# Kernel optimization log

Hardware: AMD Instinct MI355X
Metric: run time of the kernel (lower is better)

The kernel has to match this reference:

```python
import jax, jax.numpy as jnp
import numpy as np

B, S, E, H = 8, 2048, 384, 6
D = E // H  # head dim = 64


def setup_inputs() -> dict:
    key = jax.random.key(0)
    ks = jax.random.split(key, 5)
    s = 1.0 / np.sqrt(E)
    return {
        "x": jax.random.normal(ks[0], (B, S, E), dtype=jnp.float32),
        "Wq": jax.random.normal(ks[1], (E, E), dtype=jnp.float32) * s,
        "Wk": jax.random.normal(ks[2], (E, E), dtype=jnp.float32) * s,
        "Wv": jax.random.normal(ks[3], (E, E), dtype=jnp.float32) * s,
        "Wo": jax.random.normal(ks[4], (E, E), dtype=jnp.float32) * s,
        "bo": jnp.zeros((E,), dtype=jnp.float32),
    }


def reference(x, Wq, Wk, Wv, Wo, bo):
    b, s, e = x.shape
    # QKV projections (torch Linear with bias=False: x @ W.T; here W stored as [in,out])
    q = (x @ Wq).reshape(b, s, H, D).transpose(0, 2, 1, 3)  # [b,h,s,d]
    k = (x @ Wk).reshape(b, s, H, D).transpose(0, 2, 1, 3)
    v = (x @ Wv).reshape(b, s, H, D).transpose(0, 2, 1, 3)
    scores = jnp.einsum("bhqd,bhkd->bhqk", q, k) / jnp.sqrt(jnp.asarray(D, x.dtype))
    causal = jnp.tril(jnp.ones((s, s), dtype=bool))
    scores = jnp.where(causal, scores, -jnp.inf)
    attn = jax.nn.softmax(scores, axis=-1)
    # NOTE: original applies dropout but then uses the PRE-dropout softmax for @V,
    # so dropout is a no-op; we faithfully omit it.
    out = jnp.einsum("bhqk,bhkd->bhqd", attn, v)  # [b,h,s,d]
    out = out.transpose(0, 2, 1, 3).reshape(b, s, e)
    return out @ Wo + bo
```

## Files before the change

kernel.cpp:

```cpp
#include <hip/hip_runtime.h>
#include <hip/hip_bf16.h>
#include <cstdint>
#include <cstddef>

typedef __attribute__((ext_vector_type(8))) short short8;
typedef __attribute__((ext_vector_type(4))) float f32x4;

#define S_LEN 2048
#define EMB 384
#define NH 6
#define HD 64
#define NB 8
#define QSCALE 0.180336880f

__device__ __forceinline__ unsigned short f2bf(float f) {
  return __builtin_bit_cast(unsigned short, __float2bfloat16(f));
}

__global__ __launch_bounds__(256) void k_prep(
    const float* __restrict__ x, unsigned short* __restrict__ xb,
    const float* __restrict__ Wq, const float* __restrict__ Wk,
    const float* __restrict__ Wv, const float* __restrict__ Wo,
    unsigned short* __restrict__ Wqt, unsigned short* __restrict__ Wkt,
    unsigned short* __restrict__ Wvt, unsigned short* __restrict__ Wot) {
  const int tid = threadIdx.x;
  if (blockIdx.x < 1536) {
    int i = blockIdx.x * 256 + tid;
    const int n4 = (NB * S_LEN * EMB) / 4;
    for (; i < n4; i += 1536 * 256) {
      const float4 v = reinterpret_cast<const float4*>(x)[i];
      ushort4 o;
      o.x = f2bf(v.x); o.y = f2bf(v.y); o.z = f2bf(v.z); o.w = f2bf(v.w);
      reinterpret_cast<ushort4*>(xb)[i] = o;
    }
  } else {
    __shared__ unsigned short Lw[64 * 66];
    const int bx2 = blockIdx.x - 1536;
    const int mat = bx2 / 36;
    const int tile = bx2 - mat * 36;
    const int k0 = (tile / 6) * 64;
    const int n0 = (tile % 6) * 64;
    const float* W = (mat == 0) ? Wq : (mat == 1) ? Wk : (mat == 2) ? Wv : Wo;
    unsigned short* Wt = (mat == 0) ? Wqt : (mat == 1) ? Wkt : (mat == 2) ? Wvt : Wot;
    const int f4 = tid & 15;
#pragma unroll
    for (int it = 0; it < 4; ++it) {
      const int kl = it * 16 + (tid >> 4);
      const float4 v = reinterpret_cast<const float4*>(W + (size_t)(k0 + kl) * EMB + n0)[f4];
      Lw[kl * 66 + f4 * 4 + 0] = f2bf(v.x);
      Lw[kl * 66 + f4 * 4 + 1] = f2bf(v.y);
      Lw[kl * 66 + f4 * 4 + 2] = f2bf(v.z);
      Lw[kl * 66 + f4 * 4 + 3] = f2bf(v.w);
    }
    __syncthreads();
    const int g = tid & 7;
#pragma unroll
    for (int it = 0; it < 2; ++it) {
      const int nl = it * 32 + (tid >> 3);
      short8 o;
#pragma unroll
      for (int j = 0; j < 8; ++j) o[j] = (short)Lw[(g * 8 + j) * 66 + nl];
      *reinterpret_cast<short8*>(Wt + (size_t)(n0 + nl) * EMB + k0 + g * 8) = o;
    }
  }
}

__global__ __launch_bounds__(256) void k_qkv(
    const unsigned short* __restrict__ xb,
    const unsigned short* __restrict__ Wqt,
    const unsigned short* __restrict__ Wkt,
    const unsigned short* __restrict__ Wvt,
    unsigned short* __restrict__ Qb,
    unsigned short* __restrict__ Kb,
    unsigned short* __restrict__ Vtb) {
  __shared__ __attribute__((aligned(16))) unsigned short La[128 * 72];
  __shared__ __attribute__((aligned(16))) unsigned short Lt[64 * 136];

  const int tid = threadIdx.x;
  const int lane = tid & 63;
  const int w = tid >> 6;
  const int wr = w >> 1, wc = w & 1;
  const int lr = lane & 15, lg = lane >> 4;
  const int m0 = blockIdx.x * 128;
  const int wsel = blockIdx.y / 3;
  const int n0 = (blockIdx.y % 3) * 128;
  const unsigned short* Wt = (wsel == 0) ? Wqt : (wsel == 1) ? Wkt : Wvt;

  const int srow = tid >> 3;
  const int sg = tid & 7;

  f32x4 acc[4][4] = {};
  short8 st[4];
  short8 breg[2][2][4];

#pragma unroll
  for (int i = 0; i < 4; ++i)
    st[i] = *reinterpret_cast<const short8*>(
        xb + (size_t)(m0 + i * 32 + srow) * EMB + sg * 8);
#pragma unroll
  for (int kk = 0; kk < 2; ++kk)
#pragma unroll
    for (int ns = 0; ns < 4; ++ns)
      breg[0][kk][ns] = *reinterpret_cast<const short8*>(
          Wt + (size_t)(n0 + wc * 64 + ns * 16 + lr) * EMB + kk * 32 + lg * 8);

#pragma unroll
  for (int kt = 0; kt < 6; ++kt) {
    const int cur = kt & 1, nxt = cur ^ 1;
    __syncthreads();
#pragma unroll
    for (int i = 0; i < 4; ++i)
      *reinterpret_cast<short8*>(&La[(i * 32 + srow) * 72 + sg * 8]) = st[i];
    __syncthreads();
    if (kt < 5) {
      const int kn = (kt + 1) * 64;
#pragma unroll
      for (int i = 0; i < 4; ++i)
        st[i] = *reinterpret_cast<const short8*>(
            xb + (size_t)(m0 + i * 32 + srow) * EMB + kn + sg * 8);
#pragma unroll
      for (int kk = 0; kk < 2; ++kk)
#pragma unroll
        for (int ns = 0; ns < 4; ++ns)
          breg[nxt][kk][ns] = *reinterpret_cast<const short8*>(
              Wt + (size_t)(n0 + wc * 64 + ns * 16 + lr) * EMB + kn + kk * 32 + lg * 8);
    }
#pragma unroll
    for (int kk = 0; kk < 2; ++kk) {
      short8 a[4];
#pragma unroll
      for (int ms = 0; ms < 4; ++ms)
        a[ms] = *reinterpret_cast<const short8*>(
            &La[(wr * 64 + ms * 16 + lr) * 72 + kk * 32 + lg * 8]);
#pragma unroll
      for (int ms = 0; ms < 4; ++ms)
#pragma unroll
        for (int ns = 0; ns < 4; ++ns)
          acc[ms][ns] = __builtin_amdgcn_mfma_f32_16x16x32_bf16(
              a[ms], breg[cur][kk][ns], acc[ms][ns], 0, 0, 0);
    }
  }

  if (wsel != 2) {
    unsigned short* Out = (wsel == 0) ? Qb : Kb;
    const float sc = (wsel == 0) ? QSCALE : 1.0f;
#pragma unroll
    for (int ms = 0; ms < 4; ++ms)
#pragma unroll
      for (int ns = 0; ns < 4; ++ns)
#pragma unroll
        for (int r = 0; r < 4; ++r) {
          const int m = m0 + wr * 64 + ms * 16 + lg * 4 + r;
          const int n = n0 + wc * 64 + ns * 16 + lr;
          const int bb = m >> 11;
          const int s = m & 2047;
          const int h = n >> 6;
          const int d = n & 63;
          Out[(((size_t)bb * NH + h) * S_LEN + s) * HD + d] = f2bf(acc[ms][ns][r] * sc);
        }
  } else {
    const int bb = m0 >> 11;
    const int s0 = m0 & 2047;
#pragma unroll
    for (int p = 0; p < 2; ++p) {
      __syncthreads();
      if (wc == p) {
#pragma unroll
        for (int ms = 0; ms < 4; ++ms)
#pragma unroll
          for (int ns = 0; ns < 4; ++ns)
#pragma unroll
            for (int r = 0; r < 4; ++r) {
              const int dl = ns * 16 + lr;
              const int ml = wr * 64 + ms * 16 + lg * 4 + r;
              Lt[dl * 136 + (((ml >> 3) ^ (dl & 7)) << 3) + (ml & 7)] = f2bf(acc[ms][ns][r]);
            }
      }
      __syncthreads();
      const int hg = 2 * (blockIdx.y % 3) + p;
      const int c = tid & 15;
#pragma unroll
      for (int it = 0; it < 4; ++it) {
        const int d = it * 16 + (tid >> 4);
        const short8 v = *reinterpret_cast<const short8*>(
            &Lt[d * 136 + ((c ^ (d & 7)) << 3)]);
        *reinterpret_cast<short8*>(
            Vtb + (((size_t)bb * NH + hg) * HD + d) * S_LEN + s0 + c * 8) = v;
      }
    }
  }
}

__global__ __launch_bounds__(256) void k_attn(
    const unsigned short* __restrict__ Qb,
    const unsigned short* __restrict__ Kb,
    const unsigned short* __restrict__ Vtg,
    unsigned short* __restrict__ Ob) {
  __shared__ __attribute__((aligned(16))) unsigned short Ks[64 * 64];
  __shared__ __attribute__((aligned(16))) unsigned short Vt[64 * 64];
  __shared__ __attribute__((aligned(16))) unsigned short Ps[64 * 64];

  const int tid = threadIdx.x;
  const int lane = tid & 63;
  const int w = tid >> 6;
  const int lr = lane & 15, lg = lane >> 4;

  const int lin = blockIdx.x;
  const int idx = lin >> 3;
  const int bh = (lin & 7) * 6 + (idx >> 5);
  const int qt = 31 - (idx & 31);

  const unsigned short* Qp = Qb + (size_t)bh * S_LEN * HD;
  const unsigned short* Kp = Kb + (size_t)bh * S_LEN * HD;
  const unsigned short* Vp = Vtg + (size_t)bh * S_LEN * HD;
  const int b = bh / NH, hh = bh - b * NH;

  const int srow = tid >> 3;
  const int sslot = tid & 7;
  const int wsl0 = (sslot ^ (srow & 7)) << 3;

  const int qbase = qt * 64 + w * 16;

  const short8 aq0 = *reinterpret_cast<const short8*>(Qp + (size_t)(qbase + lr) * HD + lg * 8);
  const short8 aq1 = *reinterpret_cast<const short8*>(Qp + (size_t)(qbase + lr) * HD + 32 + lg * 8);

  f32x4 o[4] = {};
  float l_i[4] = {0.f, 0.f, 0.f, 0.f};

  short8 pk0 = *reinterpret_cast<const short8*>(Kp + (size_t)srow * HD + sslot * 8);
  short8 pk1 = *reinterpret_cast<const short8*>(Kp + (size_t)(srow + 32) * HD + sslot * 8);
  short8 pv0 = *reinterpret_cast<const short8*>(Vp + (size_t)srow * S_LEN + sslot * 8);
  short8 pv1 = *reinterpret_cast<const short8*>(Vp + (size_t)(srow + 32) * S_LEN + sslot * 8);

  for (int t = 0; t <= qt; ++t) {
    __syncthreads();
    *reinterpret_cast<short8*>(&Ks[srow * 64 + wsl0]) = pk0;
    *reinterpret_cast<short8*>(&Ks[(srow + 32) * 64 + wsl0]) = pk1;
    *reinterpret_cast<short8*>(&Vt[srow * 64 + wsl0]) = pv0;
    *reinterpret_cast<short8*>(&Vt[(srow + 32) * 64 + wsl0]) = pv1;
    __syncthreads();

    if (t < qt) {
      const int tn = (t + 1) * 64;
      pk0 = *reinterpret_cast<const short8*>(Kp + (size_t)(tn + srow) * HD + sslot * 8);
      pk1 = *reinterpret_cast<const short8*>(Kp + (size_t)(tn + srow + 32) * HD + sslot * 8);
      pv0 = *reinterpret_cast<const short8*>(Vp + (size_t)srow * S_LEN + tn + sslot * 8);
      pv1 = *reinterpret_cast<const short8*>(Vp + (size_t)(srow + 32) * S_LEN + tn + sslot * 8);
    }

    float sv[4][4];
    __builtin_amdgcn_s_setprio(1);
#pragma unroll
    for (int ks = 0; ks < 4; ++ks) {
      const int kstart = t * 64 + ks * 16;
      if (kstart > qbase + 15) {
#pragma unroll
        for (int r = 0; r < 4; ++r) sv[ks][r] = -1e30f;
      } else {
        const int krow = ks * 16 + lr;
        const int kx = krow & 7;
        const short8 bk0 = *reinterpret_cast<const short8*>(&Ks[krow * 64 + ((lg ^ kx) << 3)]);
        const short8 bk1 = *reinterpret_cast<const short8*>(&Ks[krow * 64 + (((4 + lg) ^ kx) << 3)]);
        f32x4 s = {};
        s = __builtin_amdgcn_mfma_f32_16x16x32_bf16(aq0, bk0, s, 0, 0, 0);
        s = __builtin_amdgcn_mfma_f32_16x16x32_bf16(aq1, bk1, s, 0, 0, 0);
        if (kstart + 15 <= qbase) {
#pragma unroll
          for (int r = 0; r < 4; ++r) sv[ks][r] = s[r];
        } else {
          const int kg = kstart + lr;
#pragma unroll
          for (int r = 0; r < 4; ++r)
            sv[ks][r] = (kg <= qbase + lg * 4 + r) ? s[r] : -1e30f;
        }
      }
    }
    __builtin_amdgcn_s_setprio(0);

#pragma unroll
    for (int r = 0; r < 4; ++r) {
      const int q = w * 16 + lg * 4 + r;
      const int qx = q & 7;
      const int abase = q * 64 + (lr & 7);
      const int sp = lr >> 3;
      float p[4];
#pragma unroll
      for (int ks = 0; ks < 4; ++ks) p[ks] = __builtin_amdgcn_exp2f(sv[ks][r]);
      l_i[r] += (p[0] + p[1]) + (p[2] + p[3]);
#pragma unroll
      for (int ks = 0; ks < 4; ++ks)
        Ps[abase + ((((ks << 1) | sp) ^ qx) << 3)] = f2bf(p[ks]);
    }

    const int qrow = w * 16 + lr;
    const int qx2 = qrow & 7;
    __builtin_amdgcn_s_setprio(1);
#pragma unroll
    for (int kk = 0; kk < 2; ++kk) {
      const short8 ap = *reinterpret_cast<const short8*>(
          &Ps[qrow * 64 + (((kk * 4 + lg) ^ qx2) << 3)]);
#pragma unroll
      for (int ns = 0; ns < 4; ++ns) {
        const int vrow = ns * 16 + lr;
        const short8 bv = *reinterpret_cast<const short8*>(
            &Vt[vrow * 64 + (((kk * 4 + lg) ^ (vrow & 7)) << 3)]);
        o[ns] = __builtin_amdgcn_mfma_f32_16x16x32_bf16(ap, bv, o[ns], 0, 0, 0);
      }
    }
    __builtin_amdgcn_s_setprio(0);
  }

#pragma unroll
  for (int r = 0; r < 4; ++r) {
    float l = l_i[r];
    l += __shfl_xor(l, 1);
    l += __shfl_xor(l, 2);
    l += __shfl_xor(l, 4);
    l += __shfl_xor(l, 8);
    l_i[r] = 1.0f / l;
  }
#pragma unroll
  for (int ns = 0; ns < 4; ++ns)
#pragma unroll
    for (int r = 0; r < 4; ++r) {
      const int qg = qbase + lg * 4 + r;
      const float val = o[ns][r] * l_i[r];
      Ob[((size_t)(b * S_LEN + qg)) * EMB + hh * HD + ns * 16 + lr] = f2bf(val);
    }
}

__global__ __launch_bounds__(256) void k_oproj(
    const unsigned short* __restrict__ Ob,
    const unsigned short* __restrict__ Wot,
    const float* __restrict__ bo,
    float* __restrict__ out) {
  __shared__ __attribute__((aligned(16))) unsigned short La[128 * 72];

  const int tid = threadIdx.x;
  const int lane = tid & 63;
  const int w = tid >> 6;
  const int wr = w >> 1, wc = w & 1;
  const int lr = lane & 15, lg = lane >> 4;
  const int m0 = blockIdx.x * 128;
  const int n0 = blockIdx.y * 128;

  const int srow = tid >> 3;
  const int sg = tid & 7;

  f32x4 acc[4][4] = {};
  short8 st[4];
  short8 breg[2][2][4];

#pragma unroll
  for (int i = 0; i < 4; ++i)
    st[i] = *reinterpret_cast<const short8*>(
        Ob + (size_t)(m0 + i * 32 + srow) * EMB + sg * 8);
#pragma unroll
  for (int kk = 0; kk < 2; ++kk)
#pragma unroll
    for (int ns = 0; ns < 4; ++ns)
      breg[0][kk][ns] = *reinterpret_cast<const short8*>(
          Wot + (size_t)(n0 + wc * 64 + ns * 16 + lr) * EMB + kk * 32 + lg * 8);

#pragma unroll
  for (int kt = 0; kt < 6; ++kt) {
    const int cur = kt & 1, nxt = cur ^ 1;
    __syncthreads();
#pragma unroll
    for (int i = 0; i < 4; ++i)
      *reinterpret_cast<short8*>(&La[(i * 32 + srow) * 72 + sg * 8]) = st[i];
    __syncthreads();
    if (kt < 5) {
      const int kn = (kt + 1) * 64;
#pragma unroll
      for (int i = 0; i < 4; ++i)
        st[i] = *reinterpret_cast<const short8*>(
            Ob + (size_t)(m0 + i * 32 + srow) * EMB + kn + sg * 8);
#pragma unroll
      for (int kk = 0; kk < 2; ++kk)
#pragma unroll
        for (int ns = 0; ns < 4; ++ns)
          breg[nxt][kk][ns] = *reinterpret_cast<const short8*>(
              Wot + (size_t)(n0 + wc * 64 + ns * 16 + lr) * EMB + kn + kk * 32 + lg * 8);
    }
#pragma unroll
    for (int kk = 0; kk < 2; ++kk) {
      short8 a[4];
#pragma unroll
      for (int ms = 0; ms < 4; ++ms)
        a[ms] = *reinterpret_cast<const short8*>(
            &La[(wr * 64 + ms * 16 + lr) * 72 + kk * 32 + lg * 8]);
#pragma unroll
      for (int ms = 0; ms < 4; ++ms)
#pragma unroll
        for (int ns = 0; ns < 4; ++ns)
          acc[ms][ns] = __builtin_amdgcn_mfma_f32_16x16x32_bf16(
              a[ms], breg[cur][kk][ns], acc[ms][ns], 0, 0, 0);
    }
  }

#pragma unroll
  for (int ms = 0; ms < 4; ++ms)
#pragma unroll
    for (int ns = 0; ns < 4; ++ns)
#pragma unroll
      for (int r = 0; r < 4; ++r) {
        const int m = m0 + wr * 64 + ms * 16 + lg * 4 + r;
        const int n = n0 + wc * 64 + ns * 16 + lr;
        out[(size_t)m * EMB + n] = acc[ms][ns][r] + bo[n];
      }
}

extern "C" void kernel_launch(void* const* d_in, const int* in_sizes, int n_in,
                              void* d_out, int out_size, void* d_ws, size_t ws_size,
                              hipStream_t stream) {
  const float* x  = (const float*)d_in[0];
  const float* Wq = (const float*)d_in[1];
  const float* Wk = (const float*)d_in[2];
  const float* Wv = (const float*)d_in[3];
  const float* Wo = (const float*)d_in[4];
  const float* bo = (const float*)d_in[5];
  float* out = (float*)d_out;

  uint8_t* ws = (uint8_t*)d_ws;
  unsigned short* xb  = (unsigned short*)(ws);
  unsigned short* Wqt = (unsigned short*)(ws + 12582912);
  unsigned short* Wkt = (unsigned short*)(ws + 12877824);
  unsigned short* Wvt = (unsigned short*)(ws + 13172736);
  unsigned short* Wot = (unsigned short*)(ws + 13467648);
  unsigned short* Qb  = (unsigned short*)(ws + 13762560);
  unsigned short* Kb  = (unsigned short*)(ws + 26345472);
  unsigned short* VT  = (unsigned short*)(ws + 38928384);
  unsigned short* Ob  = (unsigned short*)(ws + 51511296);

  hipLaunchKernelGGL(k_prep, dim3(1680), dim3(256), 0, stream,
                     x, xb, Wq, Wk, Wv, Wo, Wqt, Wkt, Wvt, Wot);
  hipLaunchKernelGGL(k_qkv, dim3(128, 9), dim3(256), 0, stream,
                     xb, Wqt, Wkt, Wvt, Qb, Kb, VT);
  hipLaunchKernelGGL(k_attn, dim3(1536), dim3(256), 0, stream, Qb, Kb, VT, Ob);
  hipLaunchKernelGGL(k_oproj, dim3(128, 3), dim3(256), 0, stream, Ob, Wot, bo, out);
}
```

Baseline: 201.8 us.

## Pair causal q-tiles per attention block and remap blocks for XCD locality

The attention kernel now processes two query tiles per block (tile i and tile 31-i). This balances causal work across 768 blocks instead of launching 1536 blocks of uneven length. Block indices in the QKV and output-projection kernels are remapped so consecutive tiles land on the same XCD, which is meant to improve L2 reuse. The output projection switches to 64-row tiles, doubling its block count for better occupancy, and the s_setprio hints are removed. Pairing halves the number of attention blocks, which could leave CUs idle at the tail, and smaller oproj tiles reload the weight tile more often.

```diff
diff --git a/kernel.cpp b/kernel.cpp
--- a/kernel.cpp
+++ b/kernel.cpp
@@ -81,9 +81,15 @@
   const int w = tid >> 6;
   const int wr = w >> 1, wc = w & 1;
   const int lr = lane & 15, lg = lane >> 4;
-  const int m0 = blockIdx.x * 128;
-  const int wsel = blockIdx.y / 3;
-  const int n0 = (blockIdx.y % 3) * 128;
+
+  const int bid = blockIdx.y * 128 + blockIdx.x;
+  const int xcd = bid & 7;
+  const int pos = bid >> 3;
+  const int bx = xcd * 16 + (pos & 15);
+  const int by = pos >> 4;
+  const int m0 = bx * 128;
+  const int wsel = by / 3;
+  const int n0 = (by % 3) * 128;
   const unsigned short* Wt = (wsel == 0) ? Wqt : (wsel == 1) ? Wkt : Wvt;
 
   const int srow = tid >> 3;
@@ -177,7 +183,7 @@
             }
       }
       __syncthreads();
-      const int hg = 2 * (blockIdx.y % 3) + p;
+      const int hg = 2 * (n0 >> 7) + p;
       const int c = tid & 15;
 #pragma unroll
       for (int it = 0; it < 4; ++it) {
@@ -205,10 +211,10 @@
   const int w = tid >> 6;
   const int lr = lane & 15, lg = lane >> 4;
 
-  const int lin = blockIdx.x;
-  const int idx = lin >> 3;
-  const int bh = (lin & 7) * 6 + (idx >> 5);
-  const int qt = 31 - (idx & 31);
+  const int lin = blockIdx.y * 16 + blockIdx.x;
+  const int swz = (lin & 7) * 96 + (lin >> 3);
+  const int pair = swz & 15;
+  const int bh = swz >> 4;
 
   const unsigned short* Qp = Qb + (size_t)bh * S_LEN * HD;
   const unsigned short* Kp = Kb + (size_t)bh * S_LEN * HD;
@@ -219,114 +225,113 @@
   const int sslot = tid & 7;
   const int wsl0 = (sslot ^ (srow & 7)) << 3;
 
-  const int qbase = qt * 64 + w * 16;
-
-  const short8 aq0 = *reinterpret_cast<const short8*>(Qp + (size_t)(qbase + lr) * HD + lg * 8);
-  const short8 aq1 = *reinterpret_cast<const short8*>(Qp + (size_t)(qbase + lr) * HD + 32 + lg * 8);
-
-  f32x4 o[4] = {};
-  float l_i[4] = {0.f, 0.f, 0.f, 0.f};
-
-  short8 pk0 = *reinterpret_cast<const short8*>(Kp + (size_t)srow * HD + sslot * 8);
-  short8 pk1 = *reinterpret_cast<const short8*>(Kp + (size_t)(srow + 32) * HD + sslot * 8);
-  short8 pv0 = *reinterpret_cast<const short8*>(Vp + (size_t)srow * S_LEN + sslot * 8);
-  short8 pv1 = *reinterpret_cast<const short8*>(Vp + (size_t)(srow + 32) * S_LEN + sslot * 8);
-
-  for (int t = 0; t <= qt; ++t) {
-    __syncthreads();
-    *reinterpret_cast<short8*>(&Ks[srow * 64 + wsl0]) = pk0;
-    *reinterpret_cast<short8*>(&Ks[(srow + 32) * 64 + wsl0]) = pk1;
-    *reinterpret_cast<short8*>(&Vt[srow * 64 + wsl0]) = pv0;
-    *reinterpret_cast<short8*>(&Vt[(srow + 32) * 64 + wsl0]) = pv1;
-    __syncthreads();
-
-    if (t < qt) {
-      const int tn = (t + 1) * 64;
-      pk0 = *reinterpret_cast<const short8*>(Kp + (size_t)(tn + srow) * HD + sslot * 8);
-      pk1 = *reinterpret_cast<const short8*>(Kp + (size_t)(tn + srow + 32) * HD + sslot * 8);
-      pv0 = *reinterpret_cast<const short8*>(Vp + (size_t)srow * S_LEN + tn + sslot * 8);
-      pv1 = *reinterpret_cast<const short8*>(Vp + (size_t)(srow + 32) * S_LEN + tn + sslot * 8);
-    }
-
-    float sv[4][4];
-    __builtin_amdgcn_s_setprio(1);
-#pragma unroll
-    for (int ks = 0; ks < 4; ++ks) {
-      const int kstart = t * 64 + ks * 16;
-      if (kstart > qbase + 15) {
-#pragma unroll
-        for (int r = 0; r < 4; ++r) sv[ks][r] = -1e30f;
-      } else {
-        const int krow = ks * 16 + lr;
-        const int kx = krow & 7;
-        const short8 bk0 = *reinterpret_cast<const short8*>(&Ks[krow * 64 + ((lg ^ kx) << 3)]);
-        const short8 bk1 = *reinterpret_cast<const short8*>(&Ks[krow * 64 + (((4 + lg) ^ kx) << 3)]);
-        f32x4 s = {};
-        s = __builtin_amdgcn_mfma_f32_16x16x32_bf16(aq0, bk0, s, 0, 0, 0);
-        s = __builtin_amdgcn_mfma_f32_16x16x32_bf16(aq1, bk1, s, 0, 0, 0);
-        if (kstart + 15 <= qbase) {
-#pragma unroll
-          for (int r = 0; r < 4; ++r) sv[ks][r] = s[r];
+  for (int phase = 0; phase < 2; ++phase) {
+    const int qt = phase ? (31 - pair) : pair;
+    const int qbase = qt * 64 + w * 16;
+
+    const short8 aq0 = *reinterpret_cast<const short8*>(Qp + (size_t)(qbase + lr) * HD + lg * 8);
+    const short8 aq1 = *reinterpret_cast<const short8*>(Qp + (size_t)(qbase + lr) * HD + 32 + lg * 8);
+
+    f32x4 o[4] = {};
+    float l_i[4] = {0.f, 0.f, 0.f, 0.f};
+
+    short8 pk0 = *reinterpret_cast<const short8*>(Kp + (size_t)srow * HD + sslot * 8);
+    short8 pk1 = *reinterpret_cast<const short8*>(Kp + (size_t)(srow + 32) * HD + sslot * 8);
+    short8 pv0 = *reinterpret_cast<const short8*>(Vp + (size_t)srow * S_LEN + sslot * 8);
+    short8 pv1 = *reinterpret_cast<const short8*>(Vp + (size_t)(srow + 32) * S_LEN + sslot * 8);
+
+    for (int t = 0; t <= qt; ++t) {
+      __syncthreads();
+      *reinterpret_cast<short8*>(&Ks[srow * 64 + wsl0]) = pk0;
+      *reinterpret_cast<short8*>(&Ks[(srow + 32) * 64 + wsl0]) = pk1;
+      *reinterpret_cast<short8*>(&Vt[srow * 64 + wsl0]) = pv0;
+      *reinterpret_cast<short8*>(&Vt[(srow + 32) * 64 + wsl0]) = pv1;
+      __syncthreads();
+
+      if (t < qt) {
+        const int tn = (t + 1) * 64;
+        pk0 = *reinterpret_cast<const short8*>(Kp + (size_t)(tn + srow) * HD + sslot * 8);
+        pk1 = *reinterpret_cast<const short8*>(Kp + (size_t)(tn + srow + 32) * HD + sslot * 8);
+        pv0 = *reinterpret_cast<const short8*>(Vp + (size_t)srow * S_LEN + tn + sslot * 8);
+        pv1 = *reinterpret_cast<const short8*>(Vp + (size_t)(srow + 32) * S_LEN + tn + sslot * 8);
+      }
+
+      float sv[4][4];
+#pragma unroll
+      for (int ks = 0; ks < 4; ++ks) {
+        const int kstart = t * 64 + ks * 16;
+        if (kstart > qbase + 15) {
+#pragma unroll
+          for (int r = 0; r < 4; ++r) sv[ks][r] = -1e30f;
         } else {
-          const int kg = kstart + lr;
-#pragma unroll
-          for (int r = 0; r < 4; ++r)
-            sv[ks][r] = (kg <= qbase + lg * 4 + r) ? s[r] : -1e30f;
+          const int krow = ks * 16 + lr;
+          const int kx = krow & 7;
+          const short8 bk0 = *reinterpret_cast<const short8*>(&Ks[krow * 64 + ((lg ^ kx) << 3)]);
+          const short8 bk1 = *reinterpret_cast<const short8*>(&Ks[krow * 64 + (((4 + lg) ^ kx) << 3)]);
+          f32x4 s = {};
+          s = __builtin_amdgcn_mfma_f32_16x16x32_bf16(aq0, bk0, s, 0, 0, 0);
+          s = __builtin_amdgcn_mfma_f32_16x16x32_bf16(aq1, bk1, s, 0, 0, 0);
+          if (kstart + 15 <= qbase) {
+#pragma unroll
+            for (int r = 0; r < 4; ++r) sv[ks][r] = s[r];
+          } else {
+            const int kg = kstart + lr;
+#pragma unroll
+            for (int r = 0; r < 4; ++r)
+              sv[ks][r] = (kg <= qbase + lg * 4 + r) ? s[r] : -1e30f;
+          }
         }
       }
-    }
-    __builtin_amdgcn_s_setprio(0);
+
+#pragma unroll
+      for (int r = 0; r < 4; ++r) {
+        const int q = w * 16 + lg * 4 + r;
+        const int qx = q & 7;
+        const int abase = q * 64 + (lr & 7);
+        const int sp = lr >> 3;
+        float p[4];
+#pragma unroll
+        for (int ks = 0; ks < 4; ++ks) p[ks] = __builtin_amdgcn_exp2f(sv[ks][r]);
+        l_i[r] += (p[0] + p[1]) + (p[2] + p[3]);
+#pragma unroll
+        for (int ks = 0; ks < 4; ++ks)
+          Ps[abase + ((((ks << 1) | sp) ^ qx) << 3)] = f2bf(p[ks]);
+      }
+
+      const int qrow = w * 16 + lr;
+      const int qx2 = qrow & 7;
+#pragma unroll
+      for (int kk = 0; kk < 2; ++kk) {
+        const short8 ap = *reinterpret_cast<const short8*>(
+            &Ps[qrow * 64 + (((kk * 4 + lg) ^ qx2) << 3)]);
+#pragma unroll
+        for (int ns = 0; ns < 4; ++ns) {
+          const int vrow = ns * 16 + lr;
+          const short8 bv = *reinterpret_cast<const short8*>(
+              &Vt[vrow * 64 + (((kk * 4 + lg) ^ (vrow & 7)) << 3)]);
+          o[ns] = __builtin_amdgcn_mfma_f32_16x16x32_bf16(ap, bv, o[ns], 0, 0, 0);
+        }
+      }
+    }
 
 #pragma unroll
     for (int r = 0; r < 4; ++r) {
-      const int q = w * 16 + lg * 4 + r;
-      const int qx = q & 7;
-      const int abase = q * 64 + (lr & 7);
-      const int sp = lr >> 3;
-      float p[4];
-#pragma unroll
-      for (int ks = 0; ks < 4; ++ks) p[ks] = __builtin_amdgcn_exp2f(sv[ks][r]);
-      l_i[r] += (p[0] + p[1]) + (p[2] + p[3]);
-#pragma unroll
-      for (int ks = 0; ks < 4; ++ks)
-        Ps[abase + ((((ks << 1) | sp) ^ qx) << 3)] = f2bf(p[ks]);
-    }
-
-    const int qrow = w * 16 + lr;
-    const int qx2 = qrow & 7;
-    __builtin_amdgcn_s_setprio(1);
-#pragma unroll
-    for (int kk = 0; kk < 2; ++kk) {
-      const short8 ap = *reinterpret_cast<const short8*>(
-          &Ps[qrow * 64 + (((kk * 4 + lg) ^ qx2) << 3)]);
-#pragma unroll
-      for (int ns = 0; ns < 4; ++ns) {
-        const int vrow = ns * 16 + lr;
-        const short8 bv = *reinterpret_cast<const short8*>(
-            &Vt[vrow * 64 + (((kk * 4 + lg) ^ (vrow & 7)) << 3)]);
-        o[ns] = __builtin_amdgcn_mfma_f32_16x16x32_bf16(ap, bv, o[ns], 0, 0, 0);
-      }
-    }
-    __builtin_amdgcn_s_setprio(0);
+      float l = l_i[r];
+      l += __shfl_xor(l, 1);
+      l += __shfl_xor(l, 2);
+      l += __shfl_xor(l, 4);
+      l += __shfl_xor(l, 8);
+      l_i[r] = 1.0f / l;
+    }
+#pragma unroll
+    for (int ns = 0; ns < 4; ++ns)
+#pragma unroll
+      for (int r = 0; r < 4; ++r) {
+        const int qg = qbase + lg * 4 + r;
+        const float val = o[ns][r] * l_i[r];
+        Ob[((size_t)(b * S_LEN + qg)) * EMB + hh * HD + ns * 16 + lr] = f2bf(val);
+      }
   }
-
-#pragma unroll
-  for (int r = 0; r < 4; ++r) {
-    float l = l_i[r];
-    l += __shfl_xor(l, 1);
-    l += __shfl_xor(l, 2);
-    l += __shfl_xor(l, 4);
-    l += __shfl_xor(l, 8);
-    l_i[r] = 1.0f / l;
-  }
-#pragma unroll
-  for (int ns = 0; ns < 4; ++ns)
-#pragma unroll
-    for (int r = 0; r < 4; ++r) {
-      const int qg = qbase + lg * 4 + r;
-      const float val = o[ns][r] * l_i[r];
-      Ob[((size_t)(b * S_LEN + qg)) * EMB + hh * HD + ns * 16 + lr] = f2bf(val);
-    }
 }
 
 __global__ __launch_bounds__(256) void k_oproj(
@@ -334,54 +339,57 @@
     const unsigned short* __restrict__ Wot,
     const float* __restrict__ bo,
     float* __restrict__ out) {
-  __shared__ __attribute__((aligned(16))) unsigned short La[128 * 72];
+  __shared__ __attribute__((aligned(16))) unsigned short La[64 * 72];
 
   const int tid = threadIdx.x;
   const int lane = tid & 63;
   const int w = tid >> 6;
-  const int wr = w >> 1, wc = w & 1;
   const int lr = lane & 15, lg = lane >> 4;
-  const int m0 = blockIdx.x * 128;
-  const int n0 = blockIdx.y * 128;
+
+  const int bid = blockIdx.y * 256 + blockIdx.x;
+  const int xcd = bid & 7;
+  const int pos = bid >> 3;
+  const int m0 = (xcd * 32 + (pos & 31)) * 64;
+  const int n0 = (pos >> 5) * 128;
 
   const int srow = tid >> 3;
   const int sg = tid & 7;
 
-  f32x4 acc[4][4] = {};
-  short8 st[4];
-  short8 breg[2][2][4];
-
-#pragma unroll
-  for (int i = 0; i < 4; ++i)
+  f32x4 acc[4][2] = {};
+  short8 st[2];
+  short8 breg[2][2][2];
+
+#pragma unroll
+  for (int i = 0; i < 2; ++i)
     st[i] = *reinterpret_cast<const short8*>(
         Ob + (size_t)(m0 + i * 32 + srow) * EMB + sg * 8);
 #pragma unroll
   for (int kk = 0; kk < 2; ++kk)
 #pragma unroll
-    for (int ns = 0; ns < 4; ++ns)
+    for (int ns = 0; ns < 2; ++ns)
       breg[0][kk][ns] = *reinterpret_cast<const short8*>(
-          Wot + (size_t)(n0 + wc * 64 + ns * 16 + lr) * EMB + kk * 32 + lg * 8);
+          Wot + (size_t)(n0 + w * 32 + ns * 16 + lr) * EMB + kk * 32 + lg * 8);
 
 #pragma unroll
   for (int kt = 0; kt < 6; ++kt) {
     const int cur = kt & 1, nxt = cur ^ 1;
     __syncthreads();
 #pragma unroll
-    for (int i = 0; i < 4; ++i)
+    for (int i = 0; i < 2; ++i)
       *reinterpret_cast<short8*>(&La[(i * 32 + srow) * 72 + sg * 8]) = st[i];
     __syncthreads();
     if (kt < 5) {
       const int kn = (kt + 1) * 64;
 #pragma unroll
-      for (int i = 0; i < 4; ++i)
+      for (int i = 0; i < 2; ++i)
         st[i] = *reinterpret_cast<const short8*>(
             Ob + (size_t)(m0 + i * 32 + srow) * EMB + kn + sg * 8);
 #pragma unroll
       for (int kk = 0; kk < 2; ++kk)
 #pragma unroll
-        for (int ns = 0; ns < 4; ++ns)
+        for (int ns = 0; ns < 2; ++ns)
           breg[nxt][kk][ns] = *reinterpret_cast<const short8*>(
-              Wot + (size_t)(n0 + wc * 64 + ns * 16 + lr) * EMB + kn + kk * 32 + lg * 8);
+              Wot + (size_t)(n0 + w * 32 + ns * 16 + lr) * EMB + kn + kk * 32 + lg * 8);
     }
 #pragma unroll
     for (int kk = 0; kk < 2; ++kk) {
@@ -389,11 +397,11 @@
 #pragma unroll
       for (int ms = 0; ms < 4; ++ms)
         a[ms] = *reinterpret_cast<const short8*>(
-            &La[(wr * 64 + ms * 16 + lr) * 72 + kk * 32 + lg * 8]);
+            &La[(ms * 16 + lr) * 72 + kk * 32 + lg * 8]);
 #pragma unroll
       for (int ms = 0; ms < 4; ++ms)
 #pragma unroll
-        for (int ns = 0; ns < 4; ++ns)
+        for (int ns = 0; ns < 2; ++ns)
           acc[ms][ns] = __builtin_amdgcn_mfma_f32_16x16x32_bf16(
               a[ms], breg[cur][kk][ns], acc[ms][ns], 0, 0, 0);
     }
@@ -402,11 +410,11 @@
 #pragma unroll
   for (int ms = 0; ms < 4; ++ms)
 #pragma unroll
-    for (int ns = 0; ns < 4; ++ns)
+    for (int ns = 0; ns < 2; ++ns)
 #pragma unroll
       for (int r = 0; r < 4; ++r) {
-        const int m = m0 + wr * 64 + ms * 16 + lg * 4 + r;
-        const int n = n0 + wc * 64 + ns * 16 + lr;
+        const int m = m0 + ms * 16 + lg * 4 + r;
+        const int n = n0 + w * 32 + ns * 16 + lr;
         out[(size_t)m * EMB + n] = acc[ms][ns][r] + bo[n];
       }
 }
@@ -437,6 +445,6 @@
                      x, xb, Wq, Wk, Wv, Wo, Wqt, Wkt, Wvt, Wot);
   hipLaunchKernelGGL(k_qkv, dim3(128, 9), dim3(256), 0, stream,
                      xb, Wqt, Wkt, Wvt, Qb, Kb, VT);
-  hipLaunchKernelGGL(k_attn, dim3(1536), dim3(256), 0, stream, Qb, Kb, VT, Ob);
-  hipLaunchKernelGGL(k_oproj, dim3(128, 3), dim3(256), 0, stream, Ob, Wot, bo, out);
-}
+  hipLaunchKernelGGL(k_attn, dim3(16, 48), dim3(256), 0, stream, Qb, Kb, VT, Ob);
+  hipLaunchKernelGGL(k_oproj, dim3(256, 3), dim3(256), 0, stream, Ob, Wot, bo, out);
+}
```

New measurement: 197.8 us. About the same (-1.9%).
